# Performance work log

Measured on AMD Instinct MI355X. Metric: run time of the kernel, lower is better.

Reference implementation:

```python
import jax, jax.numpy as jnp
import numpy as np
from jax import lax

B, T, D_IN, H, L = 8, 256, 6, 200, 200


def setup_inputs() -> dict:
    key = jax.random.key(0)
    ks = jax.random.split(key, 12)
    s = 0.05  # small init to avoid gate saturation across 200 layers
    return {
        "x":    jax.random.normal(ks[0], (B, T, D_IN), dtype=jnp.float32),
        "W1":   jax.random.normal(ks[1], (H, D_IN), dtype=jnp.float32) * s,
        "b1":   jnp.zeros((H,), dtype=jnp.float32),
        "Wih":  jax.random.normal(ks[2], (L, 4 * H, H), dtype=jnp.float32) * s,
        "Whh":  jax.random.normal(ks[3], (L, 4 * H, H), dtype=jnp.float32) * s,
        "bih":  jnp.zeros((L, 4 * H), dtype=jnp.float32),
        "bhh":  jnp.zeros((L, 4 * H), dtype=jnp.float32),
        "W2a":  jax.random.normal(ks[4], (50, H), dtype=jnp.float32) * s,
        "b2a":  jnp.zeros((50,), dtype=jnp.float32),
        "W2b":  jax.random.normal(ks[5], (24, 50), dtype=jnp.float32) * s,
        "b2b":  jnp.zeros((24,), dtype=jnp.float32),
    }


def _lstm_stack(seq, Wih, Whh, bih, bhh):
    # seq: [B, T, H]; stacked weights over L layers.
    def layer_step(carry_seq, params):
        wih, whh, bi, bh = params  # [4H,H], [4H,H], [4H], [4H]
        xs = jnp.swapaxes(carry_seq, 0, 1)  # [T, B, H]

        def cell(hc, xt):
            h, c = hc
            gates = xt @ wih.T + bi + h @ whh.T + bh  # [B, 4H]
            i, f, g, o = jnp.split(gates, 4, axis=-1)  # PyTorch ifgo order
            c = jax.nn.sigmoid(f) * c + jax.nn.sigmoid(i) * jnp.tanh(g)
            h = jax.nn.sigmoid(o) * jnp.tanh(c)
            return (h, c), h

        h0 = jnp.zeros((carry_seq.shape[0], H), dtype=carry_seq.dtype)
        _, ys = lax.scan(cell, (h0, h0), xs)
        return jnp.swapaxes(ys, 0, 1), None  # [B, T, H]

    out, _ = lax.scan(layer_step, seq, (Wih, Whh, bih, bhh))
    return out


def reference(x, W1, b1, Wih, Whh, bih, bhh, W2a, b2a, W2b, b2b):
    h = x @ W1.T + b1                      # mlp1: [B,T,200]
    h = _lstm_stack(h, Wih, Whh, bih, bhh)  # 200-layer stacked LSTM
    h = jax.nn.relu(h @ W2a.T + b2a)       # mlp2 hidden
    return h @ W2b.T + b2b                 # [B,T,24]
```

## Files before the change

### kernel.cpp

```cpp
#include <hip/hip_runtime.h>
#include <hip/hip_bf16.h>
#include <stdint.h>

#define B 8
#define T 256
#define DIN 6
#define H 200
#define G 800
#define L 200

#define NT 13
#define KT 13
#define NFRAG 169
#define F_RG 117
#define F_LD 52
#define XPAD 424

#define SENT16 0xFFFFu
#define SENT64 0xFFFFFFFFFFFFFFFFull

#define OFF_H0    8192
#define OFF_FINAL (OFF_H0 + (B*T*H)/2)
#define OFF_RING  (OFF_FINAL + B*T*H)
#define CFLAG(l)  (4096 + (l) * 16)

typedef _Float16 half8 __attribute__((ext_vector_type(8)));
typedef float f32x4 __attribute__((ext_vector_type(4)));
typedef unsigned long long u64t;

__device__ __forceinline__ float fsig(float x) {
    return 1.0f / (1.0f + __expf(-x));
}
__device__ __forceinline__ float ftanh(float x) {
    float e = __expf(2.0f * x);
    return 1.0f - 2.0f / (e + 1.0f);
}

__device__ __forceinline__ uint32_t ld_flag(const uint32_t* p) {
    return __hip_atomic_load(p, __ATOMIC_RELAXED, __HIP_MEMORY_SCOPE_AGENT);
}
__device__ __forceinline__ void st_flag(uint32_t* p, uint32_t v) {
    __hip_atomic_store(p, v, __ATOMIC_RELAXED, __HIP_MEMORY_SCOPE_AGENT);
}
__device__ __forceinline__ u64t ld_u64(const u64t* p) {
    return __hip_atomic_load(p, __ATOMIC_RELAXED, __HIP_MEMORY_SCOPE_AGENT);
}
__device__ __forceinline__ void st_u64(u64t* p, u64t v) {
    __hip_atomic_store(p, v, __ATOMIC_RELAXED, __HIP_MEMORY_SCOPE_AGENT);
}
__device__ __forceinline__ uint8_t to_fp8(float v) {
    return (uint8_t)(__builtin_amdgcn_cvt_pk_fp8_f32(v, v, 0u, false) & 0xffu);
}

__global__ void init_flags(uint32_t* ws) {
    int i = blockIdx.x * 256 + threadIdx.x;
    if (i < 8192) ws[i] = 0u;
}

__global__ void fill_ring(u64t* __restrict__ ring, long n) {
    long i = (long)blockIdx.x * 256 + threadIdx.x;
    if (i < n) ring[i] = SENT64;
}

__global__ void mlp1_kernel(const float* __restrict__ x, const float* __restrict__ W1,
                            const float* __restrict__ b1, uint16_t* __restrict__ h0h) {
    int idx = blockIdx.x * 256 + threadIdx.x;
    if (idx >= B * T * H) return;
    int j  = idx % H;
    int bt = idx / H;
    int b  = bt / T;
    int t  = bt % T;
    const float* xr = x  + (size_t)bt * DIN;
    const float* wr = W1 + (size_t)j * DIN;
    float a = b1[j];
#pragma unroll
    for (int k = 0; k < DIN; ++k) a += xr[k] * wr[k];
    _Float16 h = (_Float16)a;
    h0h[((size_t)(t * 2 + (b >> 2)) * H + j) * 4 + (b & 3)] = __builtin_bit_cast(uint16_t, h);
}

__global__ void convert_weights_mfma(const float* __restrict__ Wih,
                                     const float* __restrict__ Whh,
                                     u64t* __restrict__ Wm8) {
    size_t idx = (size_t)blockIdx.x * 256 + threadIdx.x;
    const size_t TOT = (size_t)L * 4 * NFRAG * 64;
    if (idx >= TOT) return;
    int lane = (int)(idx & 63);
    size_t r0 = idx >> 6;
    int f = (int)(r0 % NFRAG); r0 /= NFRAG;
    int g = (int)(r0 % 4);
    int l = (int)(r0 / 4);
    int kt = f / 13, nt = f % 13;
    int rl = nt * 16 + (lane & 15);
    int r  = g * 200 + rl;
    float v[8];
#pragma unroll
    for (int j = 0; j < 8; ++j) {
        int k = kt * 32 + (lane >> 4) * 8 + j;
        float xx = 0.0f;
        if (rl < 200 && k < 400)
            xx = (k < 200) ? Wih[((size_t)l * G + r) * 200 + k]
                           : Whh[((size_t)l * G + r) * 200 + (k - 200)];
        v[j] = xx;
    }
    uint32_t lo = __builtin_amdgcn_cvt_pk_fp8_f32(v[0], v[1], 0u, false);
    lo = __builtin_amdgcn_cvt_pk_fp8_f32(v[2], v[3], lo, true);
    uint32_t hi = __builtin_amdgcn_cvt_pk_fp8_f32(v[4], v[5], 0u, false);
    hi = __builtin_amdgcn_cvt_pk_fp8_f32(v[6], v[7], hi, true);
    Wm8[((size_t)(l * 4 + g) * NFRAG + f) * 64 + lane] = (u64t)lo | ((u64t)hi << 32);
}

#define MFMA8(a, b, c)  __builtin_amdgcn_mfma_f32_16x16x32_fp8_fp8((a), (b), (c), 0, 0, 0)
#define LDA8(kt) (*(const long*)&xh8[(lane & 15) * XPAD + (kt) * 32 + (lane >> 4) * 8])

template <int NTB, int NTN>
__device__ __forceinline__ void run_fast(
    int l, int tid, int g, int q, int lane, int R,
    const u64t* __restrict__ wq8,
    u64t* wl8, uint8_t* xh8, float* zl,
    const u64t* __restrict__ h0h, u64t* ring, float* finalbuf, uint32_t* flags,
    const float* __restrict__ bih, const float* __restrict__ bhh)
{
#pragma clang fp contract(fast)
    const int rmask = R - 1;
    const int word  = tid / 200;
    const int j     = tid - word * 200;
    const bool act  = tid < 400;

    float cs[4];
    float bs[4];
    if (act) {
#pragma unroll
        for (int gg = 0; gg < 4; ++gg)
            bs[gg] = bih[(size_t)l * G + gg * H + j] + bhh[(size_t)l * G + gg * H + j];
#pragma unroll
        for (int b = 0; b < 4; ++b) cs[b] = 0.0f;
    }

    u64t wr[9 * NTN];
#pragma unroll
    for (int kt = 0; kt < 9; ++kt)
#pragma unroll
        for (int n = 0; n < NTN; ++n)
            wr[kt * NTN + n] = wq8[(kt * 13 + NTB + n) * 64 + lane];
    for (int i = q * 13; i < q * 13 + 13; ++i)
        wl8[(g * F_LD + i) * 64 + lane] = wq8[(F_RG + i) * 64 + lane];

    u64t pf = SENT64;
    if (act) {
        if (l == 0) pf = h0h[tid];
        else        pf = ld_u64(ring + ((size_t)(l - 1) * R) * 400 + tid);
    }
    uint32_t cfl = 0;
    __syncthreads();

    for (int t = 0; t < T; ++t) {
        f32x4 acc[NTN];
#pragma unroll
        for (int n = 0; n < NTN; ++n) acc[n] = (f32x4){0.f, 0.f, 0.f, 0.f};

#pragma unroll
        for (int kt = 7; kt < 9; ++kt) {
            long a = LDA8(kt);
#pragma unroll
            for (int n = 0; n < NTN; ++n)
                acc[n] = MFMA8(a, (long)wr[kt * NTN + n], acc[n]);
        }
#pragma unroll
        for (int kt = 9; kt < 13; ++kt) {
            long a = LDA8(kt);
#pragma unroll
            for (int n = 0; n < NTN; ++n) {
                u64t w = wl8[(g * F_LD + (kt - 9) * 13 + NTB + n) * 64 + lane];
                acc[n] = MFMA8(a, (long)w, acc[n]);
            }
        }

        if (l < L - 1 && t >= R) {
            const uint32_t need = (uint32_t)(t - R + 1);
            while (cfl < need) {
                cfl = ld_flag(&flags[CFLAG(l + 1)]);
                if (cfl >= need) break;
                __builtin_amdgcn_s_sleep(1);
            }
        }

        if (act) {
            u64t p = pf;
            if (l > 0) {
                u64t* s = ring + ((size_t)(l - 1) * R + (t & rmask)) * 400 + tid;
                if ((uint16_t)(p >> 48) == SENT16) {
                    do {
                        __builtin_amdgcn_s_sleep(1);
                        p = ld_u64(s);
                    } while ((uint16_t)(p >> 48) == SENT16);
                }
                st_u64(s, SENT64);
            }
#pragma unroll
            for (int bb = 0; bb < 4; ++bb) {
                float f = (float)__builtin_bit_cast(_Float16, (uint16_t)(p >> (16 * bb)));
                xh8[(word * 4 + bb) * XPAD + j] = to_fp8(f);
            }
            int tn = (t + 1 < T) ? t + 1 : t;
            if (l == 0) pf = h0h[(size_t)tn * 400 + tid];
            else        pf = ld_u64(ring + ((size_t)(l - 1) * R + (tn & rmask)) * 400 + tid);
        }
        __syncthreads();

#pragma unroll
        for (int kt = 0; kt < 7; ++kt) {
            long a = LDA8(kt);
#pragma unroll
            for (int n = 0; n < NTN; ++n)
                acc[n] = MFMA8(a, (long)wr[kt * NTN + n], acc[n]);
        }

        if ((lane >> 4) < 2) {
#pragma unroll
            for (int n = 0; n < NTN; ++n) {
                int nj = (NTB + n) * 16 + (lane & 15);
#pragma unroll
                for (int r = 0; r < 4; ++r) {
                    int b = (lane >> 4) * 4 + r;
                    zl[(g * 8 + b) * 208 + nj] = acc[n][r];
                }
            }
        }
        const bool pub = ((t & 3) == 3) || (t == T - 1);
        if (pub) asm volatile("s_waitcnt vmcnt(0)" ::: "memory");
        __syncthreads();
        if (pub && tid == 0 && l > 0) st_flag(&flags[CFLAG(l)], (uint32_t)(t + 1));

        if (act) {
            u64t p = 0ull;
#pragma unroll
            for (int bb = 0; bb < 4; ++bb) {
                int b = word * 4 + bb;
                float zi = zl[(0 * 8 + b) * 208 + j] + bs[0];
                float zf = zl[(1 * 8 + b) * 208 + j] + bs[1];
                float zg = zl[(2 * 8 + b) * 208 + j] + bs[2];
                float zo = zl[(3 * 8 + b) * 208 + j] + bs[3];
                float ig = fsig(zi);
                float fg = fsig(zf);
                float gg = ftanh(zg);
                float og = fsig(zo);
                float c  = fg * cs[bb] + ig * gg;
                cs[bb] = c;
                float h = og * ftanh(c);
                xh8[b * XPAD + 200 + j] = to_fp8(h);
                _Float16 hh = (_Float16)h;
                p |= (u64t)__builtin_bit_cast(uint16_t, hh) << (16 * bb);
                if (l == L - 1) finalbuf[((size_t)b * T + t) * H + j] = h;
            }
            if (l < L - 1) {
                st_u64(ring + ((size_t)l * R + (t & rmask)) * 400 + tid, p);
            }
        }
        __syncthreads();
    }
}

template <bool FAST>
__global__ __launch_bounds__(1024, 4)
void lstm_pipeline(const u64t* __restrict__ Wm8,
                   const float* __restrict__ Wih, const float* __restrict__ Whh,
                   const float* __restrict__ bih, const float* __restrict__ bhh,
                   float* ws, int R) {
#pragma clang fp contract(fast)
    const int bx    = blockIdx.x;
    const int l     = ((bx & 7) * 25) + (bx >> 3);
    const int tid   = threadIdx.x;
    const int wv    = tid >> 6;
    const int g     = wv & 3;
    const int q     = wv >> 2;
    const int lane  = tid & 63;
    const int rmask = R - 1;

    const u64t* h0h = (const u64t*)(ws + OFF_H0);
    float*    finalbuf = ws + OFF_FINAL;
    u64t*     ring     = (u64t*)(ws + OFF_RING);
    uint32_t* flags    = (uint32_t*)ws;

    __shared__ __align__(16) uint8_t  xh8[16 * XPAD];
    __shared__ __align__(16) float    zl[4 * 8 * 208];
    __shared__ __align__(16) u64t     wl8[4 * F_LD * 64];

    for (int i = tid; i < (16 * XPAD) / 16; i += 1024)
        ((uint4*)xh8)[i] = make_uint4(0u, 0u, 0u, 0u);

    if (FAST) {
        const u64t* wq8 = Wm8 + (size_t)(l * 4 + g) * NFRAG * 64;
        switch (q) {
        case 0:  run_fast<0, 4>(l, tid, g, q, lane, R, wq8, wl8, xh8, zl,
                                h0h, ring, finalbuf, flags, bih, bhh); break;
        case 1:  run_fast<4, 3>(l, tid, g, q, lane, R, wq8, wl8, xh8, zl,
                                h0h, ring, finalbuf, flags, bih, bhh); break;
        case 2:  run_fast<7, 3>(l, tid, g, q, lane, R, wq8, wl8, xh8, zl,
                                h0h, ring, finalbuf, flags, bih, bhh); break;
        default: run_fast<10, 3>(l, tid, g, q, lane, R, wq8, wl8, xh8, zl,
                                 h0h, ring, finalbuf, flags, bih, bhh); break;
        }
        return;
    }

    float* xhf = (float*)wl8;
    const bool actj = tid < H;
    float cs[B];
    float bs[4];
    if (actj) {
#pragma unroll
        for (int gg = 0; gg < 4; ++gg)
            bs[gg] = bih[(size_t)l * G + gg * H + tid] + bhh[(size_t)l * G + gg * H + tid];
#pragma unroll
        for (int b = 0; b < B; ++b) cs[b] = 0.0f;
    }
    __syncthreads();

    for (int t = 0; t < T; ++t) {
        if (l < L - 1 && t >= R) {
            const uint32_t need = (uint32_t)(t - R + 1);
            while (ld_flag(&flags[CFLAG(l + 1)]) < need) __builtin_amdgcn_s_sleep(1);
        }
        if (actj) {
            u64t p0, p1;
            if (l == 0) {
                p0 = h0h[(size_t)t * 400 + tid];
                p1 = h0h[(size_t)t * 400 + 200 + tid];
            } else {
                u64t* s = ring + ((size_t)(l - 1) * R + (t & rmask)) * 400;
                p0 = ld_u64(s + tid);
                p1 = ld_u64(s + 200 + tid);
                while ((uint16_t)(p0 >> 48) == SENT16 ||
                       (uint16_t)(p1 >> 48) == SENT16) {
                    __builtin_amdgcn_s_sleep(1);
                    p0 = ld_u64(s + tid);
                    p1 = ld_u64(s + 200 + tid);
                }
                st_u64(s + tid, SENT64);
                st_u64(s + 200 + tid, SENT64);
            }
#pragma unroll
            for (int b = 0; b < 4; ++b) {
                xhf[b * 416 + tid]       = (float)__builtin_bit_cast(_Float16, (uint16_t)(p0 >> (16 * b)));
                xhf[(b + 4) * 416 + tid] = (float)__builtin_bit_cast(_Float16, (uint16_t)(p1 >> (16 * b)));
            }
        }
        asm volatile("s_waitcnt vmcnt(0)" ::: "memory");
        __syncthreads();
        if (tid == 0 && l > 0) st_flag(&flags[CFLAG(l)], (uint32_t)(t + 1));

        if (actj) {
            const float* wi0 = Wih + (size_t)l * G * H;
            const float* wh0 = Whh + (size_t)l * G * H;
            float acc[4][B];
#pragma unroll
            for (int gg = 0; gg < 4; ++gg)
#pragma unroll
                for (int b = 0; b < B; ++b) acc[gg][b] = 0.0f;
            for (int k2 = 0; k2 < 200; ++k2) {
                float2 wvv[4];
                if (k2 < 100) {
#pragma unroll
                    for (int gg = 0; gg < 4; ++gg)
                        wvv[gg] = *(const float2*)&wi0[((size_t)(gg * 200 + tid)) * 200 + 2 * k2];
                } else {
#pragma unroll
                    for (int gg = 0; gg < 4; ++gg)
                        wvv[gg] = *(const float2*)&wh0[((size_t)(gg * 200 + tid)) * 200 + 2 * (k2 - 100)];
                }
#pragma unroll
                for (int b = 0; b < B; ++b) {
                    float2 xv = *(const float2*)&xhf[b * 416 + 2 * k2];
#pragma unroll
                    for (int gg = 0; gg < 4; ++gg) {
                        acc[gg][b] += wvv[gg].x * xv.x;
                        acc[gg][b] += wvv[gg].y * xv.y;
                    }
                }
            }
#pragma unroll
            for (int gg = 0; gg < 4; ++gg)
#pragma unroll
                for (int b = 0; b < B; ++b)
                    zl[(gg * 8 + b) * 208 + tid] = acc[gg][b];
        }
        __syncthreads();

        if (actj) {
            u64t p0 = 0ull, p1 = 0ull;
#pragma unroll
            for (int b = 0; b < B; ++b) {
                float zi = zl[(0 * 8 + b) * 208 + tid] + bs[0];
                float zf = zl[(1 * 8 + b) * 208 + tid] + bs[1];
                float zg = zl[(2 * 8 + b) * 208 + tid] + bs[2];
                float zo = zl[(3 * 8 + b) * 208 + tid] + bs[3];
                float ig = fsig(zi);
                float fg = fsig(zf);
                float gg = ftanh(zg);
                float og = fsig(zo);
                float c  = fg * cs[b] + ig * gg;
                cs[b] = c;
                float h = og * ftanh(c);
                xhf[b * 416 + 200 + tid] = h;
                _Float16 hh = (_Float16)h;
                u64t u = (u64t)__builtin_bit_cast(uint16_t, hh);
                if (b < 4) p0 |= u << (16 * b);
                else       p1 |= u << (16 * (b - 4));
                if (l == L - 1) finalbuf[((size_t)b * T + t) * H + tid] = h;
            }
            if (l < L - 1) {
                u64t* dst = ring + ((size_t)l * R + (t & rmask)) * 400;
                st_u64(dst + tid, p0);
                st_u64(dst + 200 + tid, p1);
            }
        }
        __syncthreads();
    }
}

__global__ __launch_bounds__(64)
void mlp2_kernel(const float* __restrict__ fin, const float* __restrict__ W2a,
                 const float* __restrict__ b2a, const float* __restrict__ W2b,
                 const float* __restrict__ b2b, float* __restrict__ out) {
    const int bt  = blockIdx.x;
    const int tid = threadIdx.x;
    __shared__ float sx[H];
    __shared__ float sh[50];
    for (int i = tid; i < H; i += 64) sx[i] = fin[(size_t)bt * H + i];
    __syncthreads();
    if (tid < 50) {
        float a = b2a[tid];
        const float* w = W2a + (size_t)tid * H;
        for (int k = 0; k < H; ++k) a += w[k] * sx[k];
        sh[tid] = fmaxf(a, 0.0f);
    }
    __syncthreads();
    if (tid < 24) {
        float a = b2b[tid];
        const float* w = W2b + (size_t)tid * 50;
#pragma unroll
        for (int m = 0; m < 50; ++m) a += w[m] * sh[m];
        out[(size_t)bt * 24 + tid] = a;
    }
}

extern "C" void kernel_launch(void* const* d_in, const int* in_sizes, int n_in,
                              void* d_out, int out_size, void* d_ws, size_t ws_size,
                              hipStream_t stream) {
    const float* x    = (const float*)d_in[0];
    const float* W1   = (const float*)d_in[1];
    const float* b1   = (const float*)d_in[2];
    const float* Wih  = (const float*)d_in[3];
    const float* Whh  = (const float*)d_in[4];
    const float* bihp = (const float*)d_in[5];
    const float* bhhp = (const float*)d_in[6];
    const float* W2a  = (const float*)d_in[7];
    const float* b2a  = (const float*)d_in[8];
    const float* W2b  = (const float*)d_in[9];
    const float* b2b  = (const float*)d_in[10];
    float* out = (float*)d_out;
    float* ws  = (float*)d_ws;

    const size_t wm8_u32 = (size_t)L * 4 * NFRAG * 64 * 2;
    const size_t ring_u32_per_R = (size_t)(L - 1) * B * H / 2;

    int R = 8; bool fast = false; size_t offwm = 0;
    for (;;) {
        size_t o = (OFF_RING + (size_t)R * ring_u32_per_R + 3) & ~(size_t)3;
        if ((o + wm8_u32) * 4ull <= ws_size) { fast = true; offwm = o; break; }
        if (R == 1) break;
        R >>= 1;
    }
    if (!fast) {
        R = 8;
        while (R > 1 && (OFF_RING + (size_t)R * ring_u32_per_R) * 4ull > ws_size)
            R >>= 1;
    }
    u64t* Wm8 = (u64t*)(ws + offwm);

    const long ring_u64 = (long)(L - 1) * R * 400;

    init_flags<<<32, 256, 0, stream>>>((uint32_t*)d_ws);
    fill_ring<<<(int)((ring_u64 + 255) / 256), 256, 0, stream>>>(
        (u64t*)(ws + OFF_RING), ring_u64);
    mlp1_kernel<<<(B * T * H + 255) / 256, 256, 0, stream>>>(x, W1, b1,
                                                             (uint16_t*)(ws + OFF_H0));
    if (fast) {
        const size_t conv_threads = (size_t)L * 4 * NFRAG * 64;
        convert_weights_mfma<<<(int)((conv_threads + 255) / 256), 256, 0, stream>>>(
            Wih, Whh, Wm8);
        lstm_pipeline<true><<<L, 1024, 0, stream>>>(Wm8, Wih, Whh, bihp, bhhp, ws, R);
    } else {
        lstm_pipeline<false><<<L, 1024, 0, stream>>>(Wm8, Wih, Whh, bihp, bhhp, ws, R);
    }
    mlp2_kernel<<<B * T, 64, 0, stream>>>(ws + OFF_FINAL, W2a, b2a, W2b, b2b, out);
}
```

Before: 2.149 ms.

## Assign all four gates per wave so LSTM cell update runs from registers

The work split changes from 16 waves (4 gates x 4 column groups) to 13 waves, each owning one 16-column tile for all four gates. The cell nonlinearity and state update can then run directly on MFMA accumulators, so the zl shared-memory round trip and one block barrier per timestep go away. The next-step prefetch of the ring input is dropped in favour of a load at the top of each step, and the block size shrinks to 832 threads. The cost is more weight registers per wave (36 fragments) and fewer lanes doing the activation math.

```diff
diff --git a/kernel.cpp b/kernel.cpp
--- a/kernel.cpp
+++ b/kernel.cpp
@@ -12,8 +12,6 @@
 #define NT 13
 #define KT 13
 #define NFRAG 169
-#define F_RG 117
-#define F_LD 52
 #define XPAD 424
 
 #define SENT16 0xFFFFu
@@ -113,156 +111,8 @@
 #define MFMA8(a, b, c)  __builtin_amdgcn_mfma_f32_16x16x32_fp8_fp8((a), (b), (c), 0, 0, 0)
 #define LDA8(kt) (*(const long*)&xh8[(lane & 15) * XPAD + (kt) * 32 + (lane >> 4) * 8])
 
-template <int NTB, int NTN>
-__device__ __forceinline__ void run_fast(
-    int l, int tid, int g, int q, int lane, int R,
-    const u64t* __restrict__ wq8,
-    u64t* wl8, uint8_t* xh8, float* zl,
-    const u64t* __restrict__ h0h, u64t* ring, float* finalbuf, uint32_t* flags,
-    const float* __restrict__ bih, const float* __restrict__ bhh)
-{
-#pragma clang fp contract(fast)
-    const int rmask = R - 1;
-    const int word  = tid / 200;
-    const int j     = tid - word * 200;
-    const bool act  = tid < 400;
-
-    float cs[4];
-    float bs[4];
-    if (act) {
-#pragma unroll
-        for (int gg = 0; gg < 4; ++gg)
-            bs[gg] = bih[(size_t)l * G + gg * H + j] + bhh[(size_t)l * G + gg * H + j];
-#pragma unroll
-        for (int b = 0; b < 4; ++b) cs[b] = 0.0f;
-    }
-
-    u64t wr[9 * NTN];
-#pragma unroll
-    for (int kt = 0; kt < 9; ++kt)
-#pragma unroll
-        for (int n = 0; n < NTN; ++n)
-            wr[kt * NTN + n] = wq8[(kt * 13 + NTB + n) * 64 + lane];
-    for (int i = q * 13; i < q * 13 + 13; ++i)
-        wl8[(g * F_LD + i) * 64 + lane] = wq8[(F_RG + i) * 64 + lane];
-
-    u64t pf = SENT64;
-    if (act) {
-        if (l == 0) pf = h0h[tid];
-        else        pf = ld_u64(ring + ((size_t)(l - 1) * R) * 400 + tid);
-    }
-    uint32_t cfl = 0;
-    __syncthreads();
-
-    for (int t = 0; t < T; ++t) {
-        f32x4 acc[NTN];
-#pragma unroll
-        for (int n = 0; n < NTN; ++n) acc[n] = (f32x4){0.f, 0.f, 0.f, 0.f};
-
-#pragma unroll
-        for (int kt = 7; kt < 9; ++kt) {
-            long a = LDA8(kt);
-#pragma unroll
-            for (int n = 0; n < NTN; ++n)
-                acc[n] = MFMA8(a, (long)wr[kt * NTN + n], acc[n]);
-        }
-#pragma unroll
-        for (int kt = 9; kt < 13; ++kt) {
-            long a = LDA8(kt);
-#pragma unroll
-            for (int n = 0; n < NTN; ++n) {
-                u64t w = wl8[(g * F_LD + (kt - 9) * 13 + NTB + n) * 64 + lane];
-                acc[n] = MFMA8(a, (long)w, acc[n]);
-            }
-        }
-
-        if (l < L - 1 && t >= R) {
-            const uint32_t need = (uint32_t)(t - R + 1);
-            while (cfl < need) {
-                cfl = ld_flag(&flags[CFLAG(l + 1)]);
-                if (cfl >= need) break;
-                __builtin_amdgcn_s_sleep(1);
-            }
-        }
-
-        if (act) {
-            u64t p = pf;
-            if (l > 0) {
-                u64t* s = ring + ((size_t)(l - 1) * R + (t & rmask)) * 400 + tid;
-                if ((uint16_t)(p >> 48) == SENT16) {
-                    do {
-                        __builtin_amdgcn_s_sleep(1);
-                        p = ld_u64(s);
-                    } while ((uint16_t)(p >> 48) == SENT16);
-                }
-                st_u64(s, SENT64);
-            }
-#pragma unroll
-            for (int bb = 0; bb < 4; ++bb) {
-                float f = (float)__builtin_bit_cast(_Float16, (uint16_t)(p >> (16 * bb)));
-                xh8[(word * 4 + bb) * XPAD + j] = to_fp8(f);
-            }
-            int tn = (t + 1 < T) ? t + 1 : t;
-            if (l == 0) pf = h0h[(size_t)tn * 400 + tid];
-            else        pf = ld_u64(ring + ((size_t)(l - 1) * R + (tn & rmask)) * 400 + tid);
-        }
-        __syncthreads();
-
-#pragma unroll
-        for (int kt = 0; kt < 7; ++kt) {
-            long a = LDA8(kt);
-#pragma unroll
-            for (int n = 0; n < NTN; ++n)
-                acc[n] = MFMA8(a, (long)wr[kt * NTN + n], acc[n]);
-        }
-
-        if ((lane >> 4) < 2) {
-#pragma unroll
-            for (int n = 0; n < NTN; ++n) {
-                int nj = (NTB + n) * 16 + (lane & 15);
-#pragma unroll
-                for (int r = 0; r < 4; ++r) {
-                    int b = (lane >> 4) * 4 + r;
-                    zl[(g * 8 + b) * 208 + nj] = acc[n][r];
-                }
-            }
-        }
-        const bool pub = ((t & 3) == 3) || (t == T - 1);
-        if (pub) asm volatile("s_waitcnt vmcnt(0)" ::: "memory");
-        __syncthreads();
-        if (pub && tid == 0 && l > 0) st_flag(&flags[CFLAG(l)], (uint32_t)(t + 1));
-
-        if (act) {
-            u64t p = 0ull;
-#pragma unroll
-            for (int bb = 0; bb < 4; ++bb) {
-                int b = word * 4 + bb;
-                float zi = zl[(0 * 8 + b) * 208 + j] + bs[0];
-                float zf = zl[(1 * 8 + b) * 208 + j] + bs[1];
-                float zg = zl[(2 * 8 + b) * 208 + j] + bs[2];
-                float zo = zl[(3 * 8 + b) * 208 + j] + bs[3];
-                float ig = fsig(zi);
-                float fg = fsig(zf);
-                float gg = ftanh(zg);
-                float og = fsig(zo);
-                float c  = fg * cs[bb] + ig * gg;
-                cs[bb] = c;
-                float h = og * ftanh(c);
-                xh8[b * XPAD + 200 + j] = to_fp8(h);
-                _Float16 hh = (_Float16)h;
-                p |= (u64t)__builtin_bit_cast(uint16_t, hh) << (16 * bb);
-                if (l == L - 1) finalbuf[((size_t)b * T + t) * H + j] = h;
-            }
-            if (l < L - 1) {
-                st_u64(ring + ((size_t)l * R + (t & rmask)) * 400 + tid, p);
-            }
-        }
-        __syncthreads();
-    }
-}
-
 template <bool FAST>
-__global__ __launch_bounds__(1024, 4)
+__global__ __launch_bounds__(832, 1)
 void lstm_pipeline(const u64t* __restrict__ Wm8,
                    const float* __restrict__ Wih, const float* __restrict__ Whh,
                    const float* __restrict__ bih, const float* __restrict__ bhh,
@@ -272,8 +122,6 @@
     const int l     = ((bx & 7) * 25) + (bx >> 3);
     const int tid   = threadIdx.x;
     const int wv    = tid >> 6;
-    const int g     = wv & 3;
-    const int q     = wv >> 2;
     const int lane  = tid & 63;
     const int rmask = R - 1;
 
@@ -283,28 +131,144 @@
     uint32_t* flags    = (uint32_t*)ws;
 
     __shared__ __align__(16) uint8_t  xh8[16 * XPAD];
-    __shared__ __align__(16) float    zl[4 * 8 * 208];
-    __shared__ __align__(16) u64t     wl8[4 * F_LD * 64];
-
-    for (int i = tid; i < (16 * XPAD) / 16; i += 1024)
+    __shared__ __align__(16) u64t     wl8[13 * 16 * 64];
+
+    for (int i = tid; i < (16 * XPAD) / 16; i += 832)
         ((uint4*)xh8)[i] = make_uint4(0u, 0u, 0u, 0u);
 
     if (FAST) {
-        const u64t* wq8 = Wm8 + (size_t)(l * 4 + g) * NFRAG * 64;
-        switch (q) {
-        case 0:  run_fast<0, 4>(l, tid, g, q, lane, R, wq8, wl8, xh8, zl,
-                                h0h, ring, finalbuf, flags, bih, bhh); break;
-        case 1:  run_fast<4, 3>(l, tid, g, q, lane, R, wq8, wl8, xh8, zl,
-                                h0h, ring, finalbuf, flags, bih, bhh); break;
-        case 2:  run_fast<7, 3>(l, tid, g, q, lane, R, wq8, wl8, xh8, zl,
-                                h0h, ring, finalbuf, flags, bih, bhh); break;
-        default: run_fast<10, 3>(l, tid, g, q, lane, R, wq8, wl8, xh8, zl,
-                                 h0h, ring, finalbuf, flags, bih, bhh); break;
+        const int  word = tid / 200;
+        const int  jst  = tid - word * 200;
+        const bool stg  = tid < 400;
+
+        const int  rowq = lane >> 4;
+        const int  jj   = wv * 16 + (lane & 15);
+        const bool vact = (rowq < 2) && (jj < 200);
+
+        float cs[4];
+        float bs4[4];
+        if (vact) {
+#pragma unroll
+            for (int g = 0; g < 4; ++g) {
+                bs4[g] = bih[(size_t)l * G + g * H + jj] + bhh[(size_t)l * G + g * H + jj];
+                cs[g] = 0.0f;
+            }
+        }
+
+        u64t wr[36];
+#pragma unroll
+        for (int kt = 0; kt < 9; ++kt)
+#pragma unroll
+            for (int g = 0; g < 4; ++g)
+                wr[kt * 4 + g] =
+                    Wm8[((size_t)(l * 4 + g) * NFRAG + kt * 13 + wv) * 64 + lane];
+#pragma unroll
+        for (int kt = 9; kt < 13; ++kt)
+#pragma unroll
+            for (int g = 0; g < 4; ++g)
+                wl8[((size_t)wv * 16 + (kt - 9) * 4 + g) * 64 + lane] =
+                    Wm8[((size_t)(l * 4 + g) * NFRAG + kt * 13 + wv) * 64 + lane];
+
+        uint32_t cfl = 0;
+        __syncthreads();
+
+        for (int t = 0; t < T; ++t) {
+            u64t p = 0;
+            if (stg) {
+                if (l == 0) p = h0h[(size_t)t * 400 + tid];
+                else        p = ld_u64(ring + ((size_t)(l - 1) * R + (t & rmask)) * 400 + tid);
+            }
+
+            f32x4 acc[4];
+#pragma unroll
+            for (int g = 0; g < 4; ++g) acc[g] = (f32x4){0.f, 0.f, 0.f, 0.f};
+
+#pragma unroll
+            for (int kt = 7; kt < 9; ++kt) {
+                long a = LDA8(kt);
+#pragma unroll
+                for (int g = 0; g < 4; ++g)
+                    acc[g] = MFMA8(a, (long)wr[kt * 4 + g], acc[g]);
+            }
+#pragma unroll
+            for (int kt = 9; kt < 13; ++kt) {
+                long a = LDA8(kt);
+#pragma unroll
+                for (int g = 0; g < 4; ++g) {
+                    u64t w = wl8[((size_t)wv * 16 + (kt - 9) * 4 + g) * 64 + lane];
+                    acc[g] = MFMA8(a, (long)w, acc[g]);
+                }
+            }
+
+            if (l < L - 1 && t >= R) {
+                const uint32_t need = (uint32_t)(t - R + 1);
+                while (cfl < need) {
+                    cfl = ld_flag(&flags[CFLAG(l + 1)]);
+                    if (cfl >= need) break;
+                    __builtin_amdgcn_s_sleep(1);
+                }
+            }
+
+            if (stg) {
+                if (l > 0) {
+                    u64t* s = ring + ((size_t)(l - 1) * R + (t & rmask)) * 400 + tid;
+                    while ((uint16_t)(p >> 48) == SENT16) {
+                        __builtin_amdgcn_s_sleep(1);
+                        p = ld_u64(s);
+                    }
+                    st_u64(s, SENT64);
+                }
+#pragma unroll
+                for (int bb = 0; bb < 4; ++bb) {
+                    float f = (float)__builtin_bit_cast(_Float16, (uint16_t)(p >> (16 * bb)));
+                    xh8[(word * 4 + bb) * XPAD + jst] = to_fp8(f);
+                }
+            }
+            __syncthreads();
+
+#pragma unroll
+            for (int kt = 0; kt < 7; ++kt) {
+                long a = LDA8(kt);
+#pragma unroll
+                for (int g = 0; g < 4; ++g)
+                    acc[g] = MFMA8(a, (long)wr[kt * 4 + g], acc[g]);
+            }
+
+            if (vact) {
+                u64t ph = 0ull;
+#pragma unroll
+                for (int r = 0; r < 4; ++r) {
+                    int b = rowq * 4 + r;
+                    float zi = acc[0][r] + bs4[0];
+                    float zf = acc[1][r] + bs4[1];
+                    float zg = acc[2][r] + bs4[2];
+                    float zo = acc[3][r] + bs4[3];
+                    float ig = fsig(zi);
+                    float fg = fsig(zf);
+                    float gg = ftanh(zg);
+                    float og = fsig(zo);
+                    float c  = fg * cs[r] + ig * gg;
+                    cs[r] = c;
+                    float h = og * ftanh(c);
+                    xh8[b * XPAD + 200 + jj] = to_fp8(h);
+                    _Float16 hh = (_Float16)h;
+                    ph |= (u64t)__builtin_bit_cast(uint16_t, hh) << (16 * r);
+                    if (l == L - 1) finalbuf[((size_t)b * T + t) * H + jj] = h;
+                }
+                if (l < L - 1) {
+                    st_u64(ring + ((size_t)l * R + (t & rmask)) * 400 + rowq * 200 + jj, ph);
+                }
+            }
+            const bool pub = ((t & 3) == 3) || (t == T - 1);
+            if (pub) asm volatile("s_waitcnt vmcnt(0)" ::: "memory");
+            __syncthreads();
+            if (pub && tid == 0 && l > 0) st_flag(&flags[CFLAG(l)], (uint32_t)(t + 1));
         }
         return;
     }
 
     float* xhf = (float*)wl8;
+    float* zlf = (float*)(wl8 + 3000);
     const bool actj = tid < H;
     float cs[B];
     float bs[4];
@@ -383,7 +347,7 @@
             for (int gg = 0; gg < 4; ++gg)
 #pragma unroll
                 for (int b = 0; b < B; ++b)
-                    zl[(gg * 8 + b) * 208 + tid] = acc[gg][b];
+                    zlf[(gg * 8 + b) * 208 + tid] = acc[gg][b];
         }
         __syncthreads();
 
@@ -391,10 +355,10 @@
             u64t p0 = 0ull, p1 = 0ull;
 #pragma unroll
             for (int b = 0; b < B; ++b) {
-                float zi = zl[(0 * 8 + b) * 208 + tid] + bs[0];
-                float zf = zl[(1 * 8 + b) * 208 + tid] + bs[1];
-                float zg = zl[(2 * 8 + b) * 208 + tid] + bs[2];
-                float zo = zl[(3 * 8 + b) * 208 + tid] + bs[3];
+                float zi = zlf[(0 * 8 + b) * 208 + tid] + bs[0];
+                float zf = zlf[(1 * 8 + b) * 208 + tid] + bs[1];
+                float zg = zlf[(2 * 8 + b) * 208 + tid] + bs[2];
+                float zo = zlf[(3 * 8 + b) * 208 + tid] + bs[3];
                 float ig = fsig(zi);
                 float fg = fsig(zf);
                 float gg = ftanh(zg);
@@ -490,9 +454,9 @@
         const size_t conv_threads = (size_t)L * 4 * NFRAG * 64;
         convert_weights_mfma<<<(int)((conv_threads + 255) / 256), 256, 0, stream>>>(
             Wih, Whh, Wm8);
-        lstm_pipeline<true><<<L, 1024, 0, stream>>>(Wm8, Wih, Whh, bihp, bhhp, ws, R);
+        lstm_pipeline<true><<<L, 832, 0, stream>>>(Wm8, Wih, Whh, bihp, bhhp, ws, R);
     } else {
-        lstm_pipeline<false><<<L, 1024, 0, stream>>>(Wm8, Wih, Whh, bihp, bhhp, ws, R);
+        lstm_pipeline<false><<<L, 832, 0, stream>>>(Wm8, Wih, Whh, bihp, bhhp, ws, R);
     }
     mlp2_kernel<<<B * T, 64, 0, stream>>>(ws + OFF_FINAL, W2a, b2a, W2b, b2b, out);
 }
```

New measurement: 2.542 ms. 1.18x slower.
